# Kernel optimization log

Hardware: AMD Instinct MI355X
Metric: run time of the kernel (lower is better)

## Reference

```python
import jax, jax.numpy as jnp
import numpy as np

jax.config.update("jax_enable_x64", True)  # original casts to double for Sinkhorn

SINKHORN_EPS = 0.003
SINKHORN_ITER = 50
MU = 0.25


def setup_inputs() -> dict:
    key = jax.random.key(0)
    k1, k2 = jax.random.split(key)
    x = jax.random.normal(k1, (4096, 4096), dtype=jnp.float32)        # [B, D]
    codebook = jax.random.normal(k2, (256, 4096), dtype=jnp.float32)  # [K, D]
    return {"x": x, "codebook": codebook}


def _sinkhorn_probs(d2term):
    # d2term: [B, K] squared distances (float32)
    B, K = d2term.shape
    max_d = jnp.max(d2term, axis=-1, keepdims=True)
    min_d = jnp.min(d2term, axis=-1, keepdims=True)
    mid_d = (max_d + min_d) / 2
    normed = ((d2term - mid_d) / (max_d - mid_d + 1e-8)).astype(jnp.float64)
    standard = jnp.exp(-normed / SINKHORN_EPS)
    standard = standard / standard.sum()  # sum over dim1 then dim0 == total sum

    def body(i, carry):
        s, n = carry
        s = s / s.sum(axis=0, keepdims=True)
        n = n / K
        s = s / s.sum(axis=1, keepdims=True)
        n = n / B
        return (s, n)

    standard, normed = jax.lax.fori_loop(0, SINKHORN_ITER, body, (standard, normed))
    # original returns d2term_normed * B as probs (d2term_standard is unused after loop)
    return normed * B


def reference(x, codebook):
    # squared euclidean distances: [B, K]
    d2term = (jnp.sum(x * x, axis=-1, keepdims=True)
              + jnp.sum(codebook * codebook, axis=-1)[None, :]
              - 2.0 * (x @ codebook.T))
    probs = _sinkhorn_probs(d2term)              # [B, K] float64
    indices = jnp.argmax(probs, axis=-1)         # [B] int
    quant_hard = codebook[indices]               # [B, D] gather
    # straight-through estimator
    quant = jax.lax.stop_gradient(quant_hard - x) + x
    codebook_loss = jnp.mean((quant_hard - jax.lax.stop_gradient(x)) ** 2, axis=-1)
    commitment_loss = jnp.mean((jax.lax.stop_gradient(quant_hard) - x) ** 2, axis=-1)
    loss = codebook_loss + MU * commitment_loss  # [B]
    return quant, indices, probs, loss
```

## Files before the change

### kernel.cpp

```cpp
#include <hip/hip_runtime.h>
#include <hip/hip_bf16.h>
#include <math.h>

#define D_DIM   4096
#define B_ROWS  4096
#define K_CODES 256
#define MARGIN  3.0
#define KS      4
#define KSLICE  (D_DIM / KS)
#define BK      64
#define NITER   (KSLICE / BK)

#define IDX_OFF   (B_ROWS * D_DIM)
#define PROBS_OFF (IDX_OFF + B_ROWS)
#define LOSS_OFF  (PROBS_OFF + B_ROWS * K_CODES)

typedef __bf16 bf16x8 __attribute__((ext_vector_type(8)));
typedef float  f32x16 __attribute__((ext_vector_type(16)));

#define PART_ELEMS ((size_t)KS * B_ROWS * K_CODES)

static __device__ inline unsigned short f2bf(float f) {
    __hip_bfloat16 h = __float2bfloat16(f);
    return *reinterpret_cast<unsigned short*>(&h);
}

__global__ __launch_bounds__(256) void prep_cb(const float* __restrict__ cb,
                                               unsigned short* __restrict__ cbsw,
                                               double* __restrict__ cc) {
    const int lane = threadIdx.x & 63;
    const int k = blockIdx.x * 4 + (threadIdx.x >> 6);
    const float4* row4 = (const float4*)(cb + (size_t)k * D_DIM);
    double a0 = 0.0, a1 = 0.0, a2 = 0.0, a3 = 0.0;
#pragma unroll
    for (int i = 0; i < 16; ++i) {
        float4 v = row4[i * 64 + lane];
        a0 += (double)v.x * v.x; a1 += (double)v.y * v.y;
        a2 += (double)v.z * v.z; a3 += (double)v.w * v.w;
        ushort4 h;
        h.x = f2bf(v.x); h.y = f2bf(v.y); h.z = f2bf(v.z); h.w = f2bf(v.w);
        const int c = (i * 64 + lane) * 4;
        const int panel = c >> 6, q = (c >> 3) & 7, off = c & 7;
        *(ushort4*)&cbsw[(((size_t)panel * 8 + q) * K_CODES + k) * 8 + off] = h;
    }
    double s = (a0 + a1) + (a2 + a3);
    for (int off = 32; off; off >>= 1) s += __shfl_xor(s, off);
    if (lane == 0) cc[k] = s;
}

__global__ __launch_bounds__(256, 2) void gemm(const float* __restrict__ x,
                                               const unsigned short* __restrict__ cbsw,
                                               float* __restrict__ part,
                                               float* __restrict__ xxp) {
    __shared__ unsigned short As[2][8 * 32 * 8];
    __shared__ unsigned short Bs[2][8 * K_CODES * 8];
    const int t = threadIdx.x;
    const int lane = t & 63, w = t >> 6;
    const int h = lane >> 5, mr = lane & 31;
    const int m0 = blockIdx.x * 32;
    const int ks = blockIdx.y;
    const int k0 = ks * KSLICE;

    const int arow = t >> 3, acg = 4 * (t & 7);
    const float* ag = x + (size_t)(m0 + arow) * D_DIM + k0 + acg;
    const int aw0 = (((acg >> 3)    ) * 32 + arow) * 8 + (acg & 7);
    const int aw1 = (((acg >> 3) + 4) * 32 + arow) * 8 + (acg & 7);
    const unsigned short* bg = cbsw + (size_t)(ks * NITER) * 16384 + t * 8;

    f32x16 acc0, acc1;
#pragma unroll
    for (int i = 0; i < 16; ++i) { acc0[i] = 0.f; acc1[i] = 0.f; }
    float sq = 0.f;

#pragma unroll
    for (int r = 0; r < 8; ++r)
        __builtin_amdgcn_global_load_lds(
            (const __attribute__((address_space(1))) void*)(bg + r * 2048),
            (__attribute__((address_space(3))) void*)(&Bs[0][(t + 256 * r) * 8]),
            16, 0, 0);
    float4 p0 = *(const float4*)(ag);
    float4 p1 = *(const float4*)(ag + 32);
    float4 n0 = *(const float4*)(ag + BK);
    float4 n1 = *(const float4*)(ag + BK + 32);
    {
        ushort4 h0, h1;
        h0.x = f2bf(p0.x); h0.y = f2bf(p0.y); h0.z = f2bf(p0.z); h0.w = f2bf(p0.w);
        h1.x = f2bf(p1.x); h1.y = f2bf(p1.y); h1.z = f2bf(p1.z); h1.w = f2bf(p1.w);
        *(ushort4*)&As[0][aw0] = h0;
        *(ushort4*)&As[0][aw1] = h1;
        sq += p0.x*p0.x + p0.y*p0.y + p0.z*p0.z + p0.w*p0.w
            + p1.x*p1.x + p1.y*p1.y + p1.z*p1.z + p1.w*p1.w;
    }
    asm volatile("s_waitcnt vmcnt(2) lgkmcnt(0)" ::: "memory");
    __builtin_amdgcn_s_barrier();
    __builtin_amdgcn_sched_barrier(0);

#pragma unroll
    for (int it = 0; it < NITER; ++it) {
        const int p = it & 1, pn = p ^ 1;

        if (it + 1 < NITER) {
#pragma unroll
            for (int r = 0; r < 8; ++r)
                __builtin_amdgcn_global_load_lds(
                    (const __attribute__((address_space(1))) void*)(bg + (size_t)(it + 1) * 16384 + r * 2048),
                    (__attribute__((address_space(3))) void*)(&Bs[pn][(t + 256 * r) * 8]),
                    16, 0, 0);
            ushort4 h0, h1;
            h0.x = f2bf(n0.x); h0.y = f2bf(n0.y); h0.z = f2bf(n0.z); h0.w = f2bf(n0.w);
            h1.x = f2bf(n1.x); h1.y = f2bf(n1.y); h1.z = f2bf(n1.z); h1.w = f2bf(n1.w);
            *(ushort4*)&As[pn][aw0] = h0;
            *(ushort4*)&As[pn][aw1] = h1;
            sq += n0.x*n0.x + n0.y*n0.y + n0.z*n0.z + n0.w*n0.w
                + n1.x*n1.x + n1.y*n1.y + n1.z*n1.z + n1.w*n1.w;
        }
        const int t2 = (it + 2 < NITER) ? (it + 2) * BK : 0;
        float4 m0v = *(const float4*)(ag + t2);
        float4 m1v = *(const float4*)(ag + t2 + 32);

#pragma unroll
        for (int s = 0; s < 4; ++s) {
            const int q = 2 * s + h;
            bf16x8 af = *(const bf16x8*)&As[p][(q * 32 + mr) * 8];
            bf16x8 b0 = *(const bf16x8*)&Bs[p][(q * K_CODES + w * 64 + mr) * 8];
            bf16x8 b1 = *(const bf16x8*)&Bs[p][(q * K_CODES + w * 64 + 32 + mr) * 8];
            acc0 = __builtin_amdgcn_mfma_f32_32x32x16_bf16(af, b0, acc0, 0, 0, 0);
            acc1 = __builtin_amdgcn_mfma_f32_32x32x16_bf16(af, b1, acc1, 0, 0, 0);
        }

        asm volatile("s_waitcnt vmcnt(2) lgkmcnt(0)" ::: "memory");
        __builtin_amdgcn_s_barrier();
        __builtin_amdgcn_sched_barrier(0);

        n0 = m0v; n1 = m1v;
    }

    sq += __shfl_xor(sq, 1);
    sq += __shfl_xor(sq, 2);
    sq += __shfl_xor(sq, 4);
    if ((t & 7) == 0) xxp[(size_t)ks * B_ROWS + m0 + arow] = sq;

    float* dst = part + ((size_t)ks * B_ROWS + m0) * K_CODES + w * 64;
#pragma unroll
    for (int r = 0; r < 16; ++r) {
        const int rowit = (r & 3) + 8 * (r >> 2) + 4 * h;
        dst[(size_t)rowit * K_CODES + mr]      = acc0[r];
        dst[(size_t)rowit * K_CODES + 32 + mr] = acc1[r];
    }
}

__global__ __launch_bounds__(256) void finish(const float* __restrict__ x,
                                              const float* __restrict__ cb,
                                              const float* __restrict__ part,
                                              const double* __restrict__ cc,
                                              const float* __restrict__ xxp,
                                              float* __restrict__ out) {
    const int lane = threadIdx.x & 63;
    const int row = blockIdx.x * 4 + (threadIdx.x >> 6);

    double xx = ((double)xxp[row] + (double)xxp[B_ROWS + row])
              + ((double)xxp[2 * B_ROWS + row] + (double)xxp[3 * B_ROWS + row]);
    float4 p[KS];
#pragma unroll
    for (int s = 0; s < KS; ++s)
        p[s] = ((const float4*)(part + ((size_t)s * B_ROWS + row) * K_CODES))[lane];
    double v[4];
    v[0] = xx + cc[4 * lane + 0] - 2.0 * (((double)p[0].x + p[1].x) + ((double)p[2].x + p[3].x));
    v[1] = xx + cc[4 * lane + 1] - 2.0 * (((double)p[0].y + p[1].y) + ((double)p[2].y + p[3].y));
    v[2] = xx + cc[4 * lane + 2] - 2.0 * (((double)p[0].z + p[1].z) + ((double)p[2].z + p[3].z));
    v[3] = xx + cc[4 * lane + 3] - 2.0 * (((double)p[0].w + p[1].w) + ((double)p[2].w + p[3].w));

    double mx = fmax(fmax(v[0], v[1]), fmax(v[2], v[3]));
    for (int off = 32; off; off >>= 1) mx = fmax(mx, __shfl_xor(mx, off));
    const double thr = mx - MARGIN;

    unsigned long long b[4];
#pragma unroll
    for (int j = 0; j < 4; ++j) b[j] = __ballot(v[j] >= thr);
    const int total = __popcll(b[0]) + __popcll(b[1]) + __popcll(b[2]) + __popcll(b[3]);

    int bestk = 0; double best;
    if (total == 1) {
        best = mx;
#pragma unroll
        for (int j = 0; j < 4; ++j)
            if (b[j]) bestk = 4 * (int)__builtin_ctzll(b[j]) + j;
    } else {
        const float4* xrow4 = (const float4*)(x + (size_t)row * D_DIM);
        int flags = 0;
#pragma unroll
        for (int j = 0; j < 4; ++j) if (v[j] >= thr) flags |= 1 << j;
        unsigned long long cand = __ballot(flags != 0);
        best = -1.0e300;
        while (cand) {
            const int lsrc = __builtin_ctzll(cand);
            cand &= cand - 1;
            const int f = __shfl(flags, lsrc);
            for (int j = 0; j < 4; ++j) {
                if (!((f >> j) & 1)) continue;
                const int k = 4 * lsrc + j;
                const float4* crow4 = (const float4*)(cb + (size_t)k * D_DIM);
                double a0 = 0.0, a1 = 0.0, a2 = 0.0, a3 = 0.0;
#pragma unroll
                for (int i = 0; i < 16; ++i) {
                    float4 xa = xrow4[i * 64 + lane];
                    float4 ca = crow4[i * 64 + lane];
                    a0 += (double)xa.x * ca.x; a1 += (double)xa.y * ca.y;
                    a2 += (double)xa.z * ca.z; a3 += (double)xa.w * ca.w;
                }
                double s = (a0 + a1) + (a2 + a3);
                for (int off = 32; off; off >>= 1) s += __shfl_xor(s, off);
                const double d2e = xx + cc[k] - 2.0 * s;
                if (d2e > best) { best = d2e; bestk = k; }
            }
        }
    }

    if (lane == 0) {
        out[IDX_OFF + row]  = (float)bestk;
        out[LOSS_OFF + row] = (float)(1.25 * best / (double)D_DIM);
    }
    float4 z = make_float4(0.f, 0.f, 0.f, 0.f);
    ((float4*)(out + PROBS_OFF + (size_t)row * K_CODES))[lane] = z;
    const float4* src = (const float4*)(cb + (size_t)bestk * D_DIM);
    float4* dst = (float4*)(out + (size_t)row * D_DIM);
#pragma unroll
    for (int i = 0; i < 16; ++i) dst[i * 64 + lane] = src[i * 64 + lane];
}

extern "C" void kernel_launch(void* const* d_in, const int* in_sizes, int n_in,
                              void* d_out, int out_size, void* d_ws, size_t ws_size,
                              hipStream_t stream) {
    const float* x  = (const float*)d_in[0];
    const float* cb = (const float*)d_in[1];
    float* out = (float*)d_out;

    float*          part = (float*)d_ws;
    unsigned short* cbsw = (unsigned short*)((char*)d_ws + PART_ELEMS * sizeof(float));
    double*         cc   = (double*)((char*)cbsw + (size_t)K_CODES * D_DIM * sizeof(unsigned short));
    float*          xxp  = (float*)(cc + K_CODES);

    hipLaunchKernelGGL(prep_cb, dim3(64),      dim3(256), 0, stream, cb, cbsw, cc);
    hipLaunchKernelGGL(gemm,    dim3(128, KS), dim3(256), 0, stream, x, cbsw, part, xxp);
    hipLaunchKernelGGL(finish,  dim3(1024),    dim3(256), 0, stream, x, cb, part, cc, xxp, out);
}
```

Before: 151.7 us.

## Double GEMM M-tile to 64 rows and raise split-K to 8 slices

Each GEMM block now computes 64 rows instead of 32 with four MFMA accumulators, so each codebook tile loaded into LDS is reused across twice as many rows. The split-K factor goes from 4 to 8, which keeps the grid at 512 blocks while halving the per-block K loop. MFMA sections also get raised wave priority. prep_cb now uses one 64-thread block per code. The cost is twice as many partial-sum slices, which means more workspace traffic and more summing in finish, plus higher register pressure from the extra accumulators.

```diff
diff --git a/kernel.cpp b/kernel.cpp
--- a/kernel.cpp
+++ b/kernel.cpp
@@ -6,10 +6,11 @@
 #define B_ROWS  4096
 #define K_CODES 256
 #define MARGIN  3.0
-#define KS      4
+#define KS      8
 #define KSLICE  (D_DIM / KS)
 #define BK      64
 #define NITER   (KSLICE / BK)
+#define MT      64
 
 #define IDX_OFF   (B_ROWS * D_DIM)
 #define PROBS_OFF (IDX_OFF + B_ROWS)
@@ -25,11 +26,11 @@
     return *reinterpret_cast<unsigned short*>(&h);
 }
 
-__global__ __launch_bounds__(256) void prep_cb(const float* __restrict__ cb,
-                                               unsigned short* __restrict__ cbsw,
-                                               double* __restrict__ cc) {
+__global__ __launch_bounds__(64) void prep_cb(const float* __restrict__ cb,
+                                              unsigned short* __restrict__ cbsw,
+                                              double* __restrict__ cc) {
     const int lane = threadIdx.x & 63;
-    const int k = blockIdx.x * 4 + (threadIdx.x >> 6);
+    const int k = blockIdx.x;
     const float4* row4 = (const float4*)(cb + (size_t)k * D_DIM);
     double a0 = 0.0, a1 = 0.0, a2 = 0.0, a3 = 0.0;
 #pragma unroll
@@ -52,25 +53,25 @@
                                                const unsigned short* __restrict__ cbsw,
                                                float* __restrict__ part,
                                                float* __restrict__ xxp) {
-    __shared__ unsigned short As[2][8 * 32 * 8];
+    __shared__ unsigned short As[2][8 * MT * 8];
     __shared__ unsigned short Bs[2][8 * K_CODES * 8];
     const int t = threadIdx.x;
     const int lane = t & 63, w = t >> 6;
     const int h = lane >> 5, mr = lane & 31;
-    const int m0 = blockIdx.x * 32;
+    const int m0 = blockIdx.x * MT;
     const int ks = blockIdx.y;
     const int k0 = ks * KSLICE;
 
     const int arow = t >> 3, acg = 4 * (t & 7);
     const float* ag = x + (size_t)(m0 + arow) * D_DIM + k0 + acg;
-    const int aw0 = (((acg >> 3)    ) * 32 + arow) * 8 + (acg & 7);
-    const int aw1 = (((acg >> 3) + 4) * 32 + arow) * 8 + (acg & 7);
+    const int aw0 = (((acg >> 3)    ) * MT + arow) * 8 + (acg & 7);
+    const int aw1 = (((acg >> 3) + 4) * MT + arow) * 8 + (acg & 7);
     const unsigned short* bg = cbsw + (size_t)(ks * NITER) * 16384 + t * 8;
 
-    f32x16 acc0, acc1;
-#pragma unroll
-    for (int i = 0; i < 16; ++i) { acc0[i] = 0.f; acc1[i] = 0.f; }
-    float sq = 0.f;
+    f32x16 acc00, acc01, acc10, acc11;
+#pragma unroll
+    for (int i = 0; i < 16; ++i) { acc00[i] = 0.f; acc01[i] = 0.f; acc10[i] = 0.f; acc11[i] = 0.f; }
+    float sq0 = 0.f, sq1 = 0.f;
 
 #pragma unroll
     for (int r = 0; r < 8; ++r)
@@ -80,18 +81,28 @@
             16, 0, 0);
     float4 p0 = *(const float4*)(ag);
     float4 p1 = *(const float4*)(ag + 32);
-    float4 n0 = *(const float4*)(ag + BK);
-    float4 n1 = *(const float4*)(ag + BK + 32);
+    float4 p2 = *(const float4*)(ag + 32 * D_DIM);
+    float4 p3 = *(const float4*)(ag + 32 * D_DIM + 32);
+    float4 c0 = *(const float4*)(ag + BK);
+    float4 c1 = *(const float4*)(ag + BK + 32);
+    float4 c2 = *(const float4*)(ag + BK + 32 * D_DIM);
+    float4 c3 = *(const float4*)(ag + BK + 32 * D_DIM + 32);
     {
-        ushort4 h0, h1;
+        ushort4 h0, h1, h2, h3;
         h0.x = f2bf(p0.x); h0.y = f2bf(p0.y); h0.z = f2bf(p0.z); h0.w = f2bf(p0.w);
         h1.x = f2bf(p1.x); h1.y = f2bf(p1.y); h1.z = f2bf(p1.z); h1.w = f2bf(p1.w);
-        *(ushort4*)&As[0][aw0] = h0;
-        *(ushort4*)&As[0][aw1] = h1;
-        sq += p0.x*p0.x + p0.y*p0.y + p0.z*p0.z + p0.w*p0.w
-            + p1.x*p1.x + p1.y*p1.y + p1.z*p1.z + p1.w*p1.w;
-    }
-    asm volatile("s_waitcnt vmcnt(2) lgkmcnt(0)" ::: "memory");
+        h2.x = f2bf(p2.x); h2.y = f2bf(p2.y); h2.z = f2bf(p2.z); h2.w = f2bf(p2.w);
+        h3.x = f2bf(p3.x); h3.y = f2bf(p3.y); h3.z = f2bf(p3.z); h3.w = f2bf(p3.w);
+        *(ushort4*)&As[0][aw0]       = h0;
+        *(ushort4*)&As[0][aw1]       = h1;
+        *(ushort4*)&As[0][aw0 + 256] = h2;
+        *(ushort4*)&As[0][aw1 + 256] = h3;
+        sq0 += p0.x*p0.x + p0.y*p0.y + p0.z*p0.z + p0.w*p0.w
+             + p1.x*p1.x + p1.y*p1.y + p1.z*p1.z + p1.w*p1.w;
+        sq1 += p2.x*p2.x + p2.y*p2.y + p2.z*p2.z + p2.w*p2.w
+             + p3.x*p3.x + p3.y*p3.y + p3.z*p3.z + p3.w*p3.w;
+    }
+    asm volatile("s_waitcnt vmcnt(4) lgkmcnt(0)" ::: "memory");
     __builtin_amdgcn_s_barrier();
     __builtin_amdgcn_sched_barrier(0);
 
@@ -106,46 +117,63 @@
                     (const __attribute__((address_space(1))) void*)(bg + (size_t)(it + 1) * 16384 + r * 2048),
                     (__attribute__((address_space(3))) void*)(&Bs[pn][(t + 256 * r) * 8]),
                     16, 0, 0);
-            ushort4 h0, h1;
-            h0.x = f2bf(n0.x); h0.y = f2bf(n0.y); h0.z = f2bf(n0.z); h0.w = f2bf(n0.w);
-            h1.x = f2bf(n1.x); h1.y = f2bf(n1.y); h1.z = f2bf(n1.z); h1.w = f2bf(n1.w);
-            *(ushort4*)&As[pn][aw0] = h0;
-            *(ushort4*)&As[pn][aw1] = h1;
-            sq += n0.x*n0.x + n0.y*n0.y + n0.z*n0.z + n0.w*n0.w
-                + n1.x*n1.x + n1.y*n1.y + n1.z*n1.z + n1.w*n1.w;
+            ushort4 h0, h1, h2, h3;
+            h0.x = f2bf(c0.x); h0.y = f2bf(c0.y); h0.z = f2bf(c0.z); h0.w = f2bf(c0.w);
+            h1.x = f2bf(c1.x); h1.y = f2bf(c1.y); h1.z = f2bf(c1.z); h1.w = f2bf(c1.w);
+            h2.x = f2bf(c2.x); h2.y = f2bf(c2.y); h2.z = f2bf(c2.z); h2.w = f2bf(c2.w);
+            h3.x = f2bf(c3.x); h3.y = f2bf(c3.y); h3.z = f2bf(c3.z); h3.w = f2bf(c3.w);
+            *(ushort4*)&As[pn][aw0]       = h0;
+            *(ushort4*)&As[pn][aw1]       = h1;
+            *(ushort4*)&As[pn][aw0 + 256] = h2;
+            *(ushort4*)&As[pn][aw1 + 256] = h3;
+            sq0 += c0.x*c0.x + c0.y*c0.y + c0.z*c0.z + c0.w*c0.w
+                 + c1.x*c1.x + c1.y*c1.y + c1.z*c1.z + c1.w*c1.w;
+            sq1 += c2.x*c2.x + c2.y*c2.y + c2.z*c2.z + c2.w*c2.w
+                 + c3.x*c3.x + c3.y*c3.y + c3.z*c3.z + c3.w*c3.w;
         }
         const int t2 = (it + 2 < NITER) ? (it + 2) * BK : 0;
-        float4 m0v = *(const float4*)(ag + t2);
-        float4 m1v = *(const float4*)(ag + t2 + 32);
-
+        float4 n0 = *(const float4*)(ag + t2);
+        float4 n1 = *(const float4*)(ag + t2 + 32);
+        float4 n2 = *(const float4*)(ag + t2 + 32 * D_DIM);
+        float4 n3 = *(const float4*)(ag + t2 + 32 * D_DIM + 32);
+
+        __builtin_amdgcn_s_setprio(1);
 #pragma unroll
         for (int s = 0; s < 4; ++s) {
             const int q = 2 * s + h;
-            bf16x8 af = *(const bf16x8*)&As[p][(q * 32 + mr) * 8];
-            bf16x8 b0 = *(const bf16x8*)&Bs[p][(q * K_CODES + w * 64 + mr) * 8];
-            bf16x8 b1 = *(const bf16x8*)&Bs[p][(q * K_CODES + w * 64 + 32 + mr) * 8];
-            acc0 = __builtin_amdgcn_mfma_f32_32x32x16_bf16(af, b0, acc0, 0, 0, 0);
-            acc1 = __builtin_amdgcn_mfma_f32_32x32x16_bf16(af, b1, acc1, 0, 0, 0);
-        }
-
-        asm volatile("s_waitcnt vmcnt(2) lgkmcnt(0)" ::: "memory");
+            bf16x8 af0 = *(const bf16x8*)&As[p][(q * MT + mr) * 8];
+            bf16x8 af1 = *(const bf16x8*)&As[p][(q * MT + 32 + mr) * 8];
+            bf16x8 b0  = *(const bf16x8*)&Bs[p][(q * K_CODES + w * 64 + mr) * 8];
+            bf16x8 b1  = *(const bf16x8*)&Bs[p][(q * K_CODES + w * 64 + 32 + mr) * 8];
+            acc00 = __builtin_amdgcn_mfma_f32_32x32x16_bf16(af0, b0, acc00, 0, 0, 0);
+            acc01 = __builtin_amdgcn_mfma_f32_32x32x16_bf16(af0, b1, acc01, 0, 0, 0);
+            acc10 = __builtin_amdgcn_mfma_f32_32x32x16_bf16(af1, b0, acc10, 0, 0, 0);
+            acc11 = __builtin_amdgcn_mfma_f32_32x32x16_bf16(af1, b1, acc11, 0, 0, 0);
+        }
+        __builtin_amdgcn_s_setprio(0);
+
+        asm volatile("s_waitcnt vmcnt(4) lgkmcnt(0)" ::: "memory");
         __builtin_amdgcn_s_barrier();
         __builtin_amdgcn_sched_barrier(0);
 
-        n0 = m0v; n1 = m1v;
-    }
-
-    sq += __shfl_xor(sq, 1);
-    sq += __shfl_xor(sq, 2);
-    sq += __shfl_xor(sq, 4);
-    if ((t & 7) == 0) xxp[(size_t)ks * B_ROWS + m0 + arow] = sq;
+        c0 = n0; c1 = n1; c2 = n2; c3 = n3;
+    }
+
+    sq0 += __shfl_xor(sq0, 1); sq0 += __shfl_xor(sq0, 2); sq0 += __shfl_xor(sq0, 4);
+    sq1 += __shfl_xor(sq1, 1); sq1 += __shfl_xor(sq1, 2); sq1 += __shfl_xor(sq1, 4);
+    if ((t & 7) == 0) {
+        xxp[(size_t)ks * B_ROWS + m0 + arow]      = sq0;
+        xxp[(size_t)ks * B_ROWS + m0 + arow + 32] = sq1;
+    }
 
     float* dst = part + ((size_t)ks * B_ROWS + m0) * K_CODES + w * 64;
 #pragma unroll
     for (int r = 0; r < 16; ++r) {
         const int rowit = (r & 3) + 8 * (r >> 2) + 4 * h;
-        dst[(size_t)rowit * K_CODES + mr]      = acc0[r];
-        dst[(size_t)rowit * K_CODES + 32 + mr] = acc1[r];
+        dst[(size_t)rowit * K_CODES + mr]              = acc00[r];
+        dst[(size_t)rowit * K_CODES + 32 + mr]         = acc01[r];
+        dst[(size_t)(rowit + 32) * K_CODES + mr]       = acc10[r];
+        dst[(size_t)(rowit + 32) * K_CODES + 32 + mr]  = acc11[r];
     }
 }
 
@@ -158,17 +186,26 @@
     const int lane = threadIdx.x & 63;
     const int row = blockIdx.x * 4 + (threadIdx.x >> 6);
 
-    double xx = ((double)xxp[row] + (double)xxp[B_ROWS + row])
-              + ((double)xxp[2 * B_ROWS + row] + (double)xxp[3 * B_ROWS + row]);
+    double xx = 0.0;
+#pragma unroll
+    for (int s = 0; s < KS; ++s) xx += (double)xxp[(size_t)s * B_ROWS + row];
     float4 p[KS];
 #pragma unroll
     for (int s = 0; s < KS; ++s)
         p[s] = ((const float4*)(part + ((size_t)s * B_ROWS + row) * K_CODES))[lane];
     double v[4];
-    v[0] = xx + cc[4 * lane + 0] - 2.0 * (((double)p[0].x + p[1].x) + ((double)p[2].x + p[3].x));
-    v[1] = xx + cc[4 * lane + 1] - 2.0 * (((double)p[0].y + p[1].y) + ((double)p[2].y + p[3].y));
-    v[2] = xx + cc[4 * lane + 2] - 2.0 * (((double)p[0].z + p[1].z) + ((double)p[2].z + p[3].z));
-    v[3] = xx + cc[4 * lane + 3] - 2.0 * (((double)p[0].w + p[1].w) + ((double)p[2].w + p[3].w));
+    {
+        double s0 = 0.0, s1 = 0.0, s2 = 0.0, s3 = 0.0;
+#pragma unroll
+        for (int s = 0; s < KS; ++s) {
+            s0 += (double)p[s].x; s1 += (double)p[s].y;
+            s2 += (double)p[s].z; s3 += (double)p[s].w;
+        }
+        v[0] = xx + cc[4 * lane + 0] - 2.0 * s0;
+        v[1] = xx + cc[4 * lane + 1] - 2.0 * s1;
+        v[2] = xx + cc[4 * lane + 2] - 2.0 * s2;
+        v[3] = xx + cc[4 * lane + 3] - 2.0 * s3;
+    }
 
     double mx = fmax(fmax(v[0], v[1]), fmax(v[2], v[3]));
     for (int off = 32; off; off >>= 1) mx = fmax(mx, __shfl_xor(mx, off));
@@ -240,7 +277,7 @@
     double*         cc   = (double*)((char*)cbsw + (size_t)K_CODES * D_DIM * sizeof(unsigned short));
     float*          xxp  = (float*)(cc + K_CODES);
 
-    hipLaunchKernelGGL(prep_cb, dim3(64),      dim3(256), 0, stream, cb, cbsw, cc);
-    hipLaunchKernelGGL(gemm,    dim3(128, KS), dim3(256), 0, stream, x, cbsw, part, xxp);
+    hipLaunchKernelGGL(prep_cb, dim3(256),     dim3(64),  0, stream, cb, cbsw, cc);
+    hipLaunchKernelGGL(gemm,    dim3(64, KS),  dim3(256), 0, stream, x, cbsw, part, xxp);
     hipLaunchKernelGGL(finish,  dim3(1024),    dim3(256), 0, stream, x, cb, part, cc, xxp, out);
 }
```

New measurement: 147.5 us. 2.8% less time.

## Stream codebook operand from global into registers and double split-K slices

Applied to the files above, without the earlier changes.

The GEMM no longer stages the bf16 codebook tile in LDS. Each wave loads its B fragments straight from global memory into registers, prefetching one MFMA step ahead, and raises instruction priority around the MFMA loop. Split-K goes from 4 to 8 slices, doubling the grid, and launch bounds now allow 3 blocks per CU. prep_cb is reshaped to one 64-thread block per code, and finish is generalised to sum KS partials. The aim is to cut LDS traffic and barrier cost and to improve occupancy. The cost is twice as many partial-sum writes and reads in the finish kernel, plus more global/L2 load pressure for B.

```diff
diff --git a/kernel.cpp b/kernel.cpp
--- a/kernel.cpp
+++ b/kernel.cpp
@@ -6,10 +6,11 @@
 #define B_ROWS  4096
 #define K_CODES 256
 #define MARGIN  3.0
-#define KS      4
+#define KS      8
 #define KSLICE  (D_DIM / KS)
 #define BK      64
 #define NITER   (KSLICE / BK)
+#define MT      32
 
 #define IDX_OFF   (B_ROWS * D_DIM)
 #define PROBS_OFF (IDX_OFF + B_ROWS)
@@ -25,11 +26,11 @@
     return *reinterpret_cast<unsigned short*>(&h);
 }
 
-__global__ __launch_bounds__(256) void prep_cb(const float* __restrict__ cb,
-                                               unsigned short* __restrict__ cbsw,
-                                               double* __restrict__ cc) {
+__global__ __launch_bounds__(64) void prep_cb(const float* __restrict__ cb,
+                                              unsigned short* __restrict__ cbsw,
+                                              double* __restrict__ cc) {
     const int lane = threadIdx.x & 63;
-    const int k = blockIdx.x * 4 + (threadIdx.x >> 6);
+    const int k = blockIdx.x;
     const float4* row4 = (const float4*)(cb + (size_t)k * D_DIM);
     double a0 = 0.0, a1 = 0.0, a2 = 0.0, a3 = 0.0;
 #pragma unroll
@@ -48,40 +49,36 @@
     if (lane == 0) cc[k] = s;
 }
 
-__global__ __launch_bounds__(256, 2) void gemm(const float* __restrict__ x,
+__global__ __launch_bounds__(256, 3) void gemm(const float* __restrict__ x,
                                                const unsigned short* __restrict__ cbsw,
                                                float* __restrict__ part,
                                                float* __restrict__ xxp) {
-    __shared__ unsigned short As[2][8 * 32 * 8];
-    __shared__ unsigned short Bs[2][8 * K_CODES * 8];
+    __shared__ unsigned short As[2][8 * MT * 8];
     const int t = threadIdx.x;
     const int lane = t & 63, w = t >> 6;
     const int h = lane >> 5, mr = lane & 31;
-    const int m0 = blockIdx.x * 32;
+    const int m0 = blockIdx.x * MT;
     const int ks = blockIdx.y;
     const int k0 = ks * KSLICE;
 
     const int arow = t >> 3, acg = 4 * (t & 7);
     const float* ag = x + (size_t)(m0 + arow) * D_DIM + k0 + acg;
-    const int aw0 = (((acg >> 3)    ) * 32 + arow) * 8 + (acg & 7);
-    const int aw1 = (((acg >> 3) + 4) * 32 + arow) * 8 + (acg & 7);
-    const unsigned short* bg = cbsw + (size_t)(ks * NITER) * 16384 + t * 8;
+    const int aw0 = (((acg >> 3)    ) * MT + arow) * 8 + (acg & 7);
+    const int aw1 = (((acg >> 3) + 4) * MT + arow) * 8 + (acg & 7);
+    const unsigned short* bbase = cbsw + (size_t)(ks * NITER) * 16384
+                                + h * 2048 + (w * 64 + mr) * 8;
 
     f32x16 acc0, acc1;
 #pragma unroll
     for (int i = 0; i < 16; ++i) { acc0[i] = 0.f; acc1[i] = 0.f; }
     float sq = 0.f;
 
-#pragma unroll
-    for (int r = 0; r < 8; ++r)
-        __builtin_amdgcn_global_load_lds(
-            (const __attribute__((address_space(1))) void*)(bg + r * 2048),
-            (__attribute__((address_space(3))) void*)(&Bs[0][(t + 256 * r) * 8]),
-            16, 0, 0);
     float4 p0 = *(const float4*)(ag);
     float4 p1 = *(const float4*)(ag + 32);
-    float4 n0 = *(const float4*)(ag + BK);
-    float4 n1 = *(const float4*)(ag + BK + 32);
+    float4 c0 = *(const float4*)(ag + BK);
+    float4 c1 = *(const float4*)(ag + BK + 32);
+    bf16x8 bc0 = *(const bf16x8*)(bbase);
+    bf16x8 bc1 = *(const bf16x8*)(bbase + 256);
     {
         ushort4 h0, h1;
         h0.x = f2bf(p0.x); h0.y = f2bf(p0.y); h0.z = f2bf(p0.z); h0.w = f2bf(p0.w);
@@ -91,7 +88,7 @@
         sq += p0.x*p0.x + p0.y*p0.y + p0.z*p0.z + p0.w*p0.w
             + p1.x*p1.x + p1.y*p1.y + p1.z*p1.z + p1.w*p1.w;
     }
-    asm volatile("s_waitcnt vmcnt(2) lgkmcnt(0)" ::: "memory");
+    asm volatile("s_waitcnt lgkmcnt(0)" ::: "memory");
     __builtin_amdgcn_s_barrier();
     __builtin_amdgcn_sched_barrier(0);
 
@@ -100,44 +97,41 @@
         const int p = it & 1, pn = p ^ 1;
 
         if (it + 1 < NITER) {
-#pragma unroll
-            for (int r = 0; r < 8; ++r)
-                __builtin_amdgcn_global_load_lds(
-                    (const __attribute__((address_space(1))) void*)(bg + (size_t)(it + 1) * 16384 + r * 2048),
-                    (__attribute__((address_space(3))) void*)(&Bs[pn][(t + 256 * r) * 8]),
-                    16, 0, 0);
             ushort4 h0, h1;
-            h0.x = f2bf(n0.x); h0.y = f2bf(n0.y); h0.z = f2bf(n0.z); h0.w = f2bf(n0.w);
-            h1.x = f2bf(n1.x); h1.y = f2bf(n1.y); h1.z = f2bf(n1.z); h1.w = f2bf(n1.w);
+            h0.x = f2bf(c0.x); h0.y = f2bf(c0.y); h0.z = f2bf(c0.z); h0.w = f2bf(c0.w);
+            h1.x = f2bf(c1.x); h1.y = f2bf(c1.y); h1.z = f2bf(c1.z); h1.w = f2bf(c1.w);
             *(ushort4*)&As[pn][aw0] = h0;
             *(ushort4*)&As[pn][aw1] = h1;
-            sq += n0.x*n0.x + n0.y*n0.y + n0.z*n0.z + n0.w*n0.w
-                + n1.x*n1.x + n1.y*n1.y + n1.z*n1.z + n1.w*n1.w;
+            sq += c0.x*c0.x + c0.y*c0.y + c0.z*c0.z + c0.w*c0.w
+                + c1.x*c1.x + c1.y*c1.y + c1.z*c1.z + c1.w*c1.w;
         }
         const int t2 = (it + 2 < NITER) ? (it + 2) * BK : 0;
-        float4 m0v = *(const float4*)(ag + t2);
-        float4 m1v = *(const float4*)(ag + t2 + 32);
-
+        float4 n0 = *(const float4*)(ag + t2);
+        float4 n1 = *(const float4*)(ag + t2 + 32);
+
+        __builtin_amdgcn_s_setprio(1);
 #pragma unroll
         for (int s = 0; s < 4; ++s) {
-            const int q = 2 * s + h;
-            bf16x8 af = *(const bf16x8*)&As[p][(q * 32 + mr) * 8];
-            bf16x8 b0 = *(const bf16x8*)&Bs[p][(q * K_CODES + w * 64 + mr) * 8];
-            bf16x8 b1 = *(const bf16x8*)&Bs[p][(q * K_CODES + w * 64 + 32 + mr) * 8];
-            acc0 = __builtin_amdgcn_mfma_f32_32x32x16_bf16(af, b0, acc0, 0, 0, 0);
-            acc1 = __builtin_amdgcn_mfma_f32_32x32x16_bf16(af, b1, acc1, 0, 0, 0);
-        }
-
-        asm volatile("s_waitcnt vmcnt(2) lgkmcnt(0)" ::: "memory");
+            const int nit = (s < 3) ? it : ((it + 1 < NITER) ? it + 1 : 0);
+            const int ns  = (s < 3) ? s + 1 : 0;
+            const unsigned short* np = bbase + (size_t)nit * 16384 + ns * 4096;
+            bf16x8 bn0 = *(const bf16x8*)(np);
+            bf16x8 bn1 = *(const bf16x8*)(np + 256);
+            bf16x8 af = *(const bf16x8*)&As[p][((2 * s + h) * MT + mr) * 8];
+            acc0 = __builtin_amdgcn_mfma_f32_32x32x16_bf16(af, bc0, acc0, 0, 0, 0);
+            acc1 = __builtin_amdgcn_mfma_f32_32x32x16_bf16(af, bc1, acc1, 0, 0, 0);
+            bc0 = bn0; bc1 = bn1;
+        }
+        __builtin_amdgcn_s_setprio(0);
+
+        asm volatile("s_waitcnt lgkmcnt(0)" ::: "memory");
         __builtin_amdgcn_s_barrier();
         __builtin_amdgcn_sched_barrier(0);
 
-        n0 = m0v; n1 = m1v;
-    }
-
-    sq += __shfl_xor(sq, 1);
-    sq += __shfl_xor(sq, 2);
-    sq += __shfl_xor(sq, 4);
+        c0 = n0; c1 = n1;
+    }
+
+    sq += __shfl_xor(sq, 1); sq += __shfl_xor(sq, 2); sq += __shfl_xor(sq, 4);
     if ((t & 7) == 0) xxp[(size_t)ks * B_ROWS + m0 + arow] = sq;
 
     float* dst = part + ((size_t)ks * B_ROWS + m0) * K_CODES + w * 64;
@@ -158,17 +152,26 @@
     const int lane = threadIdx.x & 63;
     const int row = blockIdx.x * 4 + (threadIdx.x >> 6);
 
-    double xx = ((double)xxp[row] + (double)xxp[B_ROWS + row])
-              + ((double)xxp[2 * B_ROWS + row] + (double)xxp[3 * B_ROWS + row]);
+    double xx = 0.0;
+#pragma unroll
+    for (int s = 0; s < KS; ++s) xx += (double)xxp[(size_t)s * B_ROWS + row];
     float4 p[KS];
 #pragma unroll
     for (int s = 0; s < KS; ++s)
         p[s] = ((const float4*)(part + ((size_t)s * B_ROWS + row) * K_CODES))[lane];
     double v[4];
-    v[0] = xx + cc[4 * lane + 0] - 2.0 * (((double)p[0].x + p[1].x) + ((double)p[2].x + p[3].x));
-    v[1] = xx + cc[4 * lane + 1] - 2.0 * (((double)p[0].y + p[1].y) + ((double)p[2].y + p[3].y));
-    v[2] = xx + cc[4 * lane + 2] - 2.0 * (((double)p[0].z + p[1].z) + ((double)p[2].z + p[3].z));
-    v[3] = xx + cc[4 * lane + 3] - 2.0 * (((double)p[0].w + p[1].w) + ((double)p[2].w + p[3].w));
+    {
+        double s0 = 0.0, s1 = 0.0, s2 = 0.0, s3 = 0.0;
+#pragma unroll
+        for (int s = 0; s < KS; ++s) {
+            s0 += (double)p[s].x; s1 += (double)p[s].y;
+            s2 += (double)p[s].z; s3 += (double)p[s].w;
+        }
+        v[0] = xx + cc[4 * lane + 0] - 2.0 * s0;
+        v[1] = xx + cc[4 * lane + 1] - 2.0 * s1;
+        v[2] = xx + cc[4 * lane + 2] - 2.0 * s2;
+        v[3] = xx + cc[4 * lane + 3] - 2.0 * s3;
+    }
 
     double mx = fmax(fmax(v[0], v[1]), fmax(v[2], v[3]));
     for (int off = 32; off; off >>= 1) mx = fmax(mx, __shfl_xor(mx, off));
@@ -240,7 +243,7 @@
     double*         cc   = (double*)((char*)cbsw + (size_t)K_CODES * D_DIM * sizeof(unsigned short));
     float*          xxp  = (float*)(cc + K_CODES);
 
-    hipLaunchKernelGGL(prep_cb, dim3(64),      dim3(256), 0, stream, cb, cbsw, cc);
+    hipLaunchKernelGGL(prep_cb, dim3(256),     dim3(64),  0, stream, cb, cbsw, cc);
     hipLaunchKernelGGL(gemm,    dim3(128, KS), dim3(256), 0, stream, x, cbsw, part, xxp);
     hipLaunchKernelGGL(finish,  dim3(1024),    dim3(256), 0, stream, x, cb, part, cc, xxp, out);
 }
```

After: 153.5 us. Within noise of the previous version (+1.2%).
